# Kernel tuning notes

Measured on AMD Instinct MI355X. Metric: run time of the kernel, lower is better.

Reference implementation:

```python
import jax, jax.numpy as jnp
import numpy as np

B, S, D, H = 2, 2048, 512, 8
DK = D // H


def setup_inputs() -> dict:
    key = jax.random.key(0)
    ks = jax.random.split(key, 6)
    q = jax.random.normal(ks[0], (B, S, D), dtype=jnp.float32)
    k = jax.random.normal(ks[1], (B, S, D), dtype=jnp.float32)
    v = jax.random.normal(ks[2], (B, S, D), dtype=jnp.float32)
    mask = jax.random.randint(ks[3], (1, 1, S, S), 0, 2, dtype=jnp.int32)
    # nn.Linear weights [out, in]; scaled like torch default init
    Wq = jax.random.normal(ks[4], (D, D), dtype=jnp.float32) / np.sqrt(D)
    Wo = jax.random.normal(ks[5], (D, D), dtype=jnp.float32) / np.sqrt(D)
    return {"q": q, "k": k, "v": v, "mask": mask, "Wq": Wq, "Wo": Wo}


def _split_heads(x):
    # [B,S,D] -> [B,H,S,DK]
    return x.reshape(B, S, H, DK).transpose(0, 2, 1, 3)


def reference(q, k, v, mask, Wq, Wo):
    # NOTE: original module applies Wq to q, k AND v (faithful to source bug)
    query = _split_heads(q @ Wq.T)
    key_ = _split_heads(k @ Wq.T)
    value = _split_heads(v @ Wq.T)
    scores = jnp.einsum("bhqd,bhkd->bhqk", query, key_) / np.sqrt(DK).astype(np.float32)
    # original uses masked_fill_(mask==0, 1e-09) BEFORE softmax (not -inf)
    scores = jnp.where(mask == 0, jnp.float32(1e-9), scores)
    attn = jax.nn.softmax(scores, axis=-1)  # dropout p=0.0 -> identity
    x = jnp.einsum("bhqk,bhkd->bhqd", attn, value)
    x = x.transpose(0, 2, 1, 3).reshape(B, S, D)
    return x @ Wo.T
```

## Files before the change

### kernel.cpp

```cpp
#include <hip/hip_runtime.h>
#include <hip/hip_bf16.h>
#include <stdint.h>

#define S_LEN 2048
#define D_MOD 512
#define N_H   8
#define D_K   64

typedef short v8s __attribute__((ext_vector_type(8)));
typedef short v4s __attribute__((ext_vector_type(4)));
typedef float v4f __attribute__((ext_vector_type(4)));

__device__ __forceinline__ short f2bf(float f) {
  union { float f; unsigned u; } a; a.f = f;
  unsigned u = a.u;
  u += 0x7fffu + ((u >> 16) & 1u);
  return (short)(u >> 16);
}

__device__ __forceinline__ v4f mfma16(v8s a, v8s b, v4f c) {
  return __builtin_amdgcn_mfma_f32_16x16x32_bf16(a, b, c, 0, 0, 0);
}

__global__ __launch_bounds__(256) void cvt_kernel(
    const float* __restrict__ q, const float* __restrict__ k,
    const float* __restrict__ v, const float* __restrict__ Wq,
    const float* __restrict__ Wo,
    short* __restrict__ qb, short* __restrict__ kb, short* __restrict__ vb,
    short* __restrict__ Wqb, short* __restrict__ Wob)
{
  unsigned g = blockIdx.x * 256 + threadIdx.x;
  const float* src; short* dst; unsigned off;
  if (g < 524288u)        { src = q;  dst = qb;  off = g; }
  else if (g < 1048576u)  { src = k;  dst = kb;  off = g - 524288u; }
  else if (g < 1572864u)  { src = v;  dst = vb;  off = g - 1048576u; }
  else if (g < 1638400u)  { src = Wq; dst = Wqb; off = g - 1572864u; }
  else                    { src = Wo; dst = Wob; off = g - 1638400u; }
  float4 x = ((const float4*)src)[off];
  v4s p; p.x = f2bf(x.x); p.y = f2bf(x.y); p.z = f2bf(x.z); p.w = f2bf(x.w);
  ((v4s*)dst)[off] = p;
}

__global__ __launch_bounds__(256) void maskpack_kernel(
    const int* __restrict__ mask, unsigned long long* __restrict__ mp)
{
  int id = blockIdx.x * 256 + threadIdx.x;
  const int4* m4 = (const int4*)(mask + (size_t)id * 64);
  unsigned long long w = 0ull;
#pragma unroll
  for (int j = 0; j < 16; j++) {
    int4 v = m4[j];
    w |= (unsigned long long)(v.x != 0) << (j * 4 + 0);
    w |= (unsigned long long)(v.y != 0) << (j * 4 + 1);
    w |= (unsigned long long)(v.z != 0) << (j * 4 + 2);
    w |= (unsigned long long)(v.w != 0) << (j * 4 + 3);
  }
  mp[id] = w;
}

__global__ __launch_bounds__(256) void proj_kernel(
    const short* __restrict__ qb, const short* __restrict__ kb,
    const short* __restrict__ vb, const short* __restrict__ Wqb,
    short* __restrict__ QP, short* __restrict__ KP, short* __restrict__ VT)
{
  const int z = blockIdx.z;
  const short* __restrict__ A = (z == 0) ? qb : ((z == 1) ? kb : vb);
  const int m0 = blockIdx.x * 64, n0 = blockIdx.y * 64;
  const int tid = threadIdx.x;
  const int wave = tid >> 6, lane = tid & 63;
  const int quad = lane >> 4, l15 = lane & 15;
  const int wm = wave >> 1, wn = wave & 1;
  __shared__ short As[64][72];
  __shared__ short Bs[64][72];
  v4f acc[2][2];
#pragma unroll
  for (int i = 0; i < 2; i++)
#pragma unroll
    for (int j = 0; j < 2; j++) acc[i][j] = (v4f){0.f, 0.f, 0.f, 0.f};

  v8s a8[2], b8[2];
#pragma unroll
  for (int i = 0; i < 2; i++) {
    int fi = tid + i * 256, r = fi >> 3, c = (fi & 7) << 3;
    a8[i] = *(const v8s*)&A[(m0 + r) * 512 + c];
    b8[i] = *(const v8s*)&Wqb[(n0 + r) * 512 + c];
  }

  for (int kk = 0; kk < 512; kk += 64) {
    __syncthreads();
#pragma unroll
    for (int i = 0; i < 2; i++) {
      int fi = tid + i * 256, r = fi >> 3, c = (fi & 7) << 3;
      *(v8s*)&As[r][c] = a8[i];
      *(v8s*)&Bs[r][c] = b8[i];
    }
    __syncthreads();
    if (kk + 64 < 512) {
#pragma unroll
      for (int i = 0; i < 2; i++) {
        int fi = tid + i * 256, r = fi >> 3, c = (fi & 7) << 3;
        a8[i] = *(const v8s*)&A[(m0 + r) * 512 + kk + 64 + c];
        b8[i] = *(const v8s*)&Wqb[(n0 + r) * 512 + kk + 64 + c];
      }
    }
#pragma unroll
    for (int ms = 0; ms < 2; ms++)
#pragma unroll
      for (int ns = 0; ns < 2; ns++)
#pragma unroll
        for (int ks = 0; ks < 2; ks++) {
          union { v8s v; v4s h2[2]; } a, bb;
          a.h2[0]  = *(const v4s*)&As[wm * 32 + ms * 16 + l15][ks * 32 + quad * 8];
          a.h2[1]  = *(const v4s*)&As[wm * 32 + ms * 16 + l15][ks * 32 + quad * 8 + 4];
          bb.h2[0] = *(const v4s*)&Bs[wn * 32 + ns * 16 + l15][ks * 32 + quad * 8];
          bb.h2[1] = *(const v4s*)&Bs[wn * 32 + ns * 16 + l15][ks * 32 + quad * 8 + 4];
          acc[ms][ns] = mfma16(a.v, bb.v, acc[ms][ns]);
        }
  }
#pragma unroll
  for (int ms = 0; ms < 2; ms++)
#pragma unroll
    for (int ns = 0; ns < 2; ns++) {
      int mb = m0 + wm * 32 + ms * 16 + quad * 4;
      int n  = n0 + wn * 32 + ns * 16 + l15;
      int bI = mb >> 11, s = mb & 2047, hh = n >> 6, dk = n & 63;
      if (z == 2) {
        v4s pv;
        pv.x = f2bf(acc[ms][ns][0]); pv.y = f2bf(acc[ms][ns][1]);
        pv.z = f2bf(acc[ms][ns][2]); pv.w = f2bf(acc[ms][ns][3]);
        *(v4s*)&VT[((bI * N_H + hh) * D_K + dk) * S_LEN + s] = pv;
      } else {
        short* dst = (z == 0) ? QP : KP;
#pragma unroll
        for (int r = 0; r < 4; r++)
          dst[((bI * N_H + hh) * S_LEN + (s + r)) * D_K + dk] = f2bf(acc[ms][ns][r]);
      }
    }
}

__global__ __launch_bounds__(512, 4) void attn_kernel(
    const short* __restrict__ QP, const short* __restrict__ KP,
    const short* __restrict__ VT, const unsigned long long* __restrict__ mp,
    short* __restrict__ XP)
{
  const int h = blockIdx.y, b = blockIdx.z;
  const int tid = threadIdx.x;
  const int wave = tid >> 6;
  const int half = wave >> 2;
  const int wq   = wave & 3;
  const int lane = tid & 63;
  const int quad = lane >> 4, l15 = lane & 15;
  const short* Qh = QP + ((b * N_H + h) * S_LEN) * D_K;
  const short* Kh = KP + ((b * N_H + h) * S_LEN) * D_K;
  const short* Vh = VT + ((b * N_H + h) * D_K) * S_LEN;

  __shared__ char smem[54272];
  short* Ks = (short*)smem + half * 4608;
  short* Vs = (short*)(smem + 18432) + half * 4608;
  short* Pl = (short*)(smem + 36864) + wave * 1088;
  float* CB = (float*)smem;

  const int qrow = blockIdx.x * 64 + wq * 16;
  const int t8   = tid & 255;
  const int srow = t8 >> 2;
  const int sc   = (t8 & 3) * 8;
  const int ch0  = half * 1024;

  v8s aQ[2];
#pragma unroll
  for (int ks = 0; ks < 2; ks++)
    aQ[ks] = *(const v8s*)&Qh[(qrow + l15) * D_K + ks * 32 + quad * 8];

  const float MASKP = 3.3546263e-4f;
  const v8s ONES = {16256,16256,16256,16256,16256,16256,16256,16256};
  v4f accX[4], accL = (v4f){0.f, 0.f, 0.f, 0.f};
#pragma unroll
  for (int t = 0; t < 4; t++) accX[t] = (v4f){0.f, 0.f, 0.f, 0.f};

  v8s kreg0 = *(const v8s*)&Kh[(ch0 + srow) * D_K + sc];
  v8s kreg1 = *(const v8s*)&Kh[(ch0 + srow) * D_K + sc + 32];
  v8s vreg0 = *(const v8s*)&Vh[srow * S_LEN + ch0 + sc];
  v8s vreg1 = *(const v8s*)&Vh[srow * S_LEN + ch0 + sc + 32];
  unsigned long long mwc[4], mwn[4];
#pragma unroll
  for (int r = 0; r < 4; r++)
    mwc[r] = mp[(qrow + quad * 4 + r) * 32 + half * 16];

  for (int kt = 0; kt < 16; kt++) {
    __syncthreads();
    *(v8s*)&Ks[srow * 72 + sc]      = kreg0;
    *(v8s*)&Ks[srow * 72 + sc + 32] = kreg1;
    *(v8s*)&Vs[srow * 72 + sc]      = vreg0;
    *(v8s*)&Vs[srow * 72 + sc + 32] = vreg1;
    __syncthreads();

    if (kt + 1 < 16) {
      const int c1 = ch0 + (kt + 1) * 64;
      kreg0 = *(const v8s*)&Kh[(c1 + srow) * D_K + sc];
      kreg1 = *(const v8s*)&Kh[(c1 + srow) * D_K + sc + 32];
      vreg0 = *(const v8s*)&Vh[srow * S_LEN + c1 + sc];
      vreg1 = *(const v8s*)&Vh[srow * S_LEN + c1 + sc + 32];
#pragma unroll
      for (int r = 0; r < 4; r++)
        mwn[r] = mp[(qrow + quad * 4 + r) * 32 + half * 16 + kt + 1];
    }

#pragma unroll
    for (int t = 0; t < 4; t++) {
      v4f s = (v4f){0.f, 0.f, 0.f, 0.f};
#pragma unroll
      for (int ks = 0; ks < 2; ks++) {
        v8s bK = *(const v8s*)&Ks[(t * 16 + l15) * 72 + ks * 32 + quad * 8];
        s = mfma16(aQ[ks], bK, s);
      }
#pragma unroll
      for (int r = 0; r < 4; r++) {
        int bit = (int)((mwc[r] >> (t * 16 + l15)) & 1ull);
        float p = bit ? __expf(fmaf(s[r], 0.125f, -8.0f)) : MASKP;
        Pl[(quad * 4 + r) * 68 + t * 16 + l15] = f2bf(p);
      }
    }

    union { v8s v; v4s h2[2]; } aP[2];
#pragma unroll
    for (int ks = 0; ks < 2; ks++) {
      aP[ks].h2[0] = *(const v4s*)&Pl[l15 * 68 + ks * 32 + quad * 8];
      aP[ks].h2[1] = *(const v4s*)&Pl[l15 * 68 + ks * 32 + quad * 8 + 4];
    }
#pragma unroll
    for (int t = 0; t < 4; t++)
#pragma unroll
      for (int ks = 0; ks < 2; ks++) {
        v8s bV = *(const v8s*)&Vs[(t * 16 + l15) * 72 + ks * 32 + quad * 8];
        accX[t] = mfma16(aP[ks].v, bV, accX[t]);
      }
    accL = mfma16(aP[0].v, ONES, accL);
    accL = mfma16(aP[1].v, ONES, accL);

#pragma unroll
    for (int r = 0; r < 4; r++) mwc[r] = mwn[r];
  }

  __syncthreads();
  if (half == 1) {
    float* c = CB + (wq * 64 + lane) * 21;
#pragma unroll
    for (int t = 0; t < 4; t++)
#pragma unroll
      for (int r = 0; r < 4; r++) c[t * 4 + r] = accX[t][r];
#pragma unroll
    for (int r = 0; r < 4; r++) c[16 + r] = accL[r];
  }
  __syncthreads();
  if (half == 0) {
    const float* c = CB + (wq * 64 + lane) * 21;
#pragma unroll
    for (int t = 0; t < 4; t++)
#pragma unroll
      for (int r = 0; r < 4; r++) accX[t][r] += c[t * 4 + r];
    float linv[4];
#pragma unroll
    for (int r = 0; r < 4; r++) linv[r] = 1.0f / (accL[r] + c[16 + r]);
#pragma unroll
    for (int t = 0; t < 4; t++)
#pragma unroll
      for (int r = 0; r < 4; r++) {
        float x = accX[t][r] * linv[r];
        int srw = qrow + quad * 4 + r;
        XP[(b * S_LEN + srw) * D_MOD + h * D_K + t * 16 + l15] = f2bf(x);
      }
  }
}

__global__ __launch_bounds__(256) void outproj_kernel(
    const short* __restrict__ XP, const short* __restrict__ Wob,
    float* __restrict__ out)
{
  const int m0 = blockIdx.x * 64, n0 = blockIdx.y * 64;
  const int tid = threadIdx.x;
  const int wave = tid >> 6, lane = tid & 63;
  const int quad = lane >> 4, l15 = lane & 15;
  const int wm = wave >> 1, wn = wave & 1;
  __shared__ short As[64][72];
  __shared__ short Bs[64][72];
  v4f acc[2][2];
#pragma unroll
  for (int i = 0; i < 2; i++)
#pragma unroll
    for (int j = 0; j < 2; j++) acc[i][j] = (v4f){0.f, 0.f, 0.f, 0.f};

  v8s a8[2], b8[2];
#pragma unroll
  for (int i = 0; i < 2; i++) {
    int fi = tid + i * 256, r = fi >> 3, c = (fi & 7) << 3;
    a8[i] = *(const v8s*)&XP[(m0 + r) * 512 + c];
    b8[i] = *(const v8s*)&Wob[(n0 + r) * 512 + c];
  }

  for (int kk = 0; kk < 512; kk += 64) {
    __syncthreads();
#pragma unroll
    for (int i = 0; i < 2; i++) {
      int fi = tid + i * 256, r = fi >> 3, c = (fi & 7) << 3;
      *(v8s*)&As[r][c] = a8[i];
      *(v8s*)&Bs[r][c] = b8[i];
    }
    __syncthreads();
    if (kk + 64 < 512) {
#pragma unroll
      for (int i = 0; i < 2; i++) {
        int fi = tid + i * 256, r = fi >> 3, c = (fi & 7) << 3;
        a8[i] = *(const v8s*)&XP[(m0 + r) * 512 + kk + 64 + c];
        b8[i] = *(const v8s*)&Wob[(n0 + r) * 512 + kk + 64 + c];
      }
    }
#pragma unroll
    for (int ms = 0; ms < 2; ms++)
#pragma unroll
      for (int ns = 0; ns < 2; ns++)
#pragma unroll
        for (int ks = 0; ks < 2; ks++) {
          union { v8s v; v4s h2[2]; } a, bb;
          a.h2[0]  = *(const v4s*)&As[wm * 32 + ms * 16 + l15][ks * 32 + quad * 8];
          a.h2[1]  = *(const v4s*)&As[wm * 32 + ms * 16 + l15][ks * 32 + quad * 8 + 4];
          bb.h2[0] = *(const v4s*)&Bs[wn * 32 + ns * 16 + l15][ks * 32 + quad * 8];
          bb.h2[1] = *(const v4s*)&Bs[wn * 32 + ns * 16 + l15][ks * 32 + quad * 8 + 4];
          acc[ms][ns] = mfma16(a.v, bb.v, acc[ms][ns]);
        }
  }
#pragma unroll
  for (int ms = 0; ms < 2; ms++)
#pragma unroll
    for (int ns = 0; ns < 2; ns++) {
      int n = n0 + wn * 32 + ns * 16 + l15;
#pragma unroll
      for (int r = 0; r < 4; r++) {
        int m = m0 + wm * 32 + ms * 16 + quad * 4 + r;
        out[m * 512 + n] = acc[ms][ns][r];
      }
    }
}

extern "C" void kernel_launch(void* const* d_in, const int* in_sizes, int n_in,
                              void* d_out, int out_size, void* d_ws, size_t ws_size,
                              hipStream_t stream) {
  const float* q  = (const float*)d_in[0];
  const float* k  = (const float*)d_in[1];
  const float* v  = (const float*)d_in[2];
  const int* mask = (const int*)d_in[3];
  const float* Wq = (const float*)d_in[4];
  const float* Wo = (const float*)d_in[5];
  float* out = (float*)d_out;
  char* ws = (char*)d_ws;
  short* QP = (short*)(ws);
  short* KP = (short*)(ws + (4u << 20));
  short* VT = (short*)(ws + (8u << 20));
  short* XP = (short*)(ws + (12u << 20));
  unsigned long long* MP = (unsigned long long*)(ws + (16u << 20));
  short* qb  = (short*)(ws + (17u << 20));
  short* kb  = (short*)(ws + (21u << 20));
  short* vb  = (short*)(ws + (25u << 20));
  short* Wqb = (short*)(ws + (29u << 20));
  short* Wob = (short*)(ws + (29u << 20) + (512u << 10));

  cvt_kernel<<<dim3(6656), 256, 0, stream>>>(q, k, v, Wq, Wo, qb, kb, vb, Wqb, Wob);
  maskpack_kernel<<<dim3(256), 256, 0, stream>>>(mask, MP);
  proj_kernel<<<dim3(64, 8, 3), 256, 0, stream>>>(qb, kb, vb, Wqb, QP, KP, VT);
  attn_kernel<<<dim3(32, N_H, 2), 512, 0, stream>>>(QP, KP, VT, MP, XP);
  outproj_kernel<<<dim3(64, 8, 1), 256, 0, stream>>>(XP, Wob, out);
}
```

Baseline: 159.7 us.

## Keep softmax probabilities in registers via transposed QK MFMA and merge prep kernels

The attention kernel now computes S^T by swapping the MFMA operands. Each lane therefore holds the probabilities in the layout needed as the A operand of a 16x16x16 bf16 MFMA for the PV product. This removes the per-wave LDS round trip for P. The row sum moves from an MFMA against a ones vector to a scalar accumulation plus cross-lane shuffles, and LDS usage shrinks. Separately, the conversion and mask-packing kernels are merged into a single launch; the trade-off is more, smaller MFMA instructions for PV.

New measurement: 163.8 us. 2.6% more time.

```diff
diff --git a/kernel.cpp b/kernel.cpp
--- a/kernel.cpp
+++ b/kernel.cpp
@@ -21,41 +21,44 @@
 __device__ __forceinline__ v4f mfma16(v8s a, v8s b, v4f c) {
   return __builtin_amdgcn_mfma_f32_16x16x32_bf16(a, b, c, 0, 0, 0);
 }
-
-__global__ __launch_bounds__(256) void cvt_kernel(
+__device__ __forceinline__ v4f mfma16x16(v4s a, v4s b, v4f c) {
+  return __builtin_amdgcn_mfma_f32_16x16x16bf16_1k(a, b, c, 0, 0, 0);
+}
+
+__global__ __launch_bounds__(256) void prep_kernel(
     const float* __restrict__ q, const float* __restrict__ k,
     const float* __restrict__ v, const float* __restrict__ Wq,
-    const float* __restrict__ Wo,
+    const float* __restrict__ Wo, const int* __restrict__ mask,
     short* __restrict__ qb, short* __restrict__ kb, short* __restrict__ vb,
-    short* __restrict__ Wqb, short* __restrict__ Wob)
+    short* __restrict__ Wqb, short* __restrict__ Wob,
+    unsigned long long* __restrict__ mp)
 {
-  unsigned g = blockIdx.x * 256 + threadIdx.x;
-  const float* src; short* dst; unsigned off;
-  if (g < 524288u)        { src = q;  dst = qb;  off = g; }
-  else if (g < 1048576u)  { src = k;  dst = kb;  off = g - 524288u; }
-  else if (g < 1572864u)  { src = v;  dst = vb;  off = g - 1048576u; }
-  else if (g < 1638400u)  { src = Wq; dst = Wqb; off = g - 1572864u; }
-  else                    { src = Wo; dst = Wob; off = g - 1638400u; }
-  float4 x = ((const float4*)src)[off];
-  v4s p; p.x = f2bf(x.x); p.y = f2bf(x.y); p.z = f2bf(x.z); p.w = f2bf(x.w);
-  ((v4s*)dst)[off] = p;
-}
-
-__global__ __launch_bounds__(256) void maskpack_kernel(
-    const int* __restrict__ mask, unsigned long long* __restrict__ mp)
-{
-  int id = blockIdx.x * 256 + threadIdx.x;
-  const int4* m4 = (const int4*)(mask + (size_t)id * 64);
-  unsigned long long w = 0ull;
-#pragma unroll
-  for (int j = 0; j < 16; j++) {
-    int4 v = m4[j];
-    w |= (unsigned long long)(v.x != 0) << (j * 4 + 0);
-    w |= (unsigned long long)(v.y != 0) << (j * 4 + 1);
-    w |= (unsigned long long)(v.z != 0) << (j * 4 + 2);
-    w |= (unsigned long long)(v.w != 0) << (j * 4 + 3);
-  }
-  mp[id] = w;
+  unsigned bx = blockIdx.x;
+  if (bx < 6656u) {
+    unsigned g = bx * 256 + threadIdx.x;
+    const float* src; short* dst; unsigned off;
+    if (g < 524288u)        { src = q;  dst = qb;  off = g; }
+    else if (g < 1048576u)  { src = k;  dst = kb;  off = g - 524288u; }
+    else if (g < 1572864u)  { src = v;  dst = vb;  off = g - 1048576u; }
+    else if (g < 1638400u)  { src = Wq; dst = Wqb; off = g - 1572864u; }
+    else                    { src = Wo; dst = Wob; off = g - 1638400u; }
+    float4 x = ((const float4*)src)[off];
+    v4s p; p.x = f2bf(x.x); p.y = f2bf(x.y); p.z = f2bf(x.z); p.w = f2bf(x.w);
+    ((v4s*)dst)[off] = p;
+  } else {
+    int id = (bx - 6656u) * 256 + threadIdx.x;
+    const int4* m4 = (const int4*)(mask + (size_t)id * 64);
+    unsigned long long w = 0ull;
+#pragma unroll
+    for (int j = 0; j < 16; j++) {
+      int4 mv = m4[j];
+      w |= (unsigned long long)(mv.x != 0) << (j * 4 + 0);
+      w |= (unsigned long long)(mv.y != 0) << (j * 4 + 1);
+      w |= (unsigned long long)(mv.z != 0) << (j * 4 + 2);
+      w |= (unsigned long long)(mv.w != 0) << (j * 4 + 3);
+    }
+    mp[id] = w;
+  }
 }
 
 __global__ __launch_bounds__(256) void proj_kernel(
@@ -154,10 +157,9 @@
   const short* Kh = KP + ((b * N_H + h) * S_LEN) * D_K;
   const short* Vh = VT + ((b * N_H + h) * D_K) * S_LEN;
 
-  __shared__ char smem[54272];
+  __shared__ char smem[36864];
   short* Ks = (short*)smem + half * 4608;
   short* Vs = (short*)(smem + 18432) + half * 4608;
-  short* Pl = (short*)(smem + 36864) + wave * 1088;
   float* CB = (float*)smem;
 
   const int qrow = blockIdx.x * 64 + wq * 16;
@@ -172,19 +174,17 @@
     aQ[ks] = *(const v8s*)&Qh[(qrow + l15) * D_K + ks * 32 + quad * 8];
 
   const float MASKP = 3.3546263e-4f;
-  const v8s ONES = {16256,16256,16256,16256,16256,16256,16256,16256};
-  v4f accX[4], accL = (v4f){0.f, 0.f, 0.f, 0.f};
-#pragma unroll
-  for (int t = 0; t < 4; t++) accX[t] = (v4f){0.f, 0.f, 0.f, 0.f};
+  float lacc = 0.f;
+  v4f accX[4];
+#pragma unroll
+  for (int u = 0; u < 4; u++) accX[u] = (v4f){0.f, 0.f, 0.f, 0.f};
 
   v8s kreg0 = *(const v8s*)&Kh[(ch0 + srow) * D_K + sc];
   v8s kreg1 = *(const v8s*)&Kh[(ch0 + srow) * D_K + sc + 32];
   v8s vreg0 = *(const v8s*)&Vh[srow * S_LEN + ch0 + sc];
   v8s vreg1 = *(const v8s*)&Vh[srow * S_LEN + ch0 + sc + 32];
-  unsigned long long mwc[4], mwn[4];
-#pragma unroll
-  for (int r = 0; r < 4; r++)
-    mwc[r] = mp[(qrow + quad * 4 + r) * 32 + half * 16];
+  unsigned long long mwc = mp[(qrow + l15) * 32 + half * 16];
+  unsigned long long mwn = 0ull;
 
   for (int kt = 0; kt < 16; kt++) {
     __syncthreads();
@@ -200,74 +200,73 @@
       kreg1 = *(const v8s*)&Kh[(c1 + srow) * D_K + sc + 32];
       vreg0 = *(const v8s*)&Vh[srow * S_LEN + c1 + sc];
       vreg1 = *(const v8s*)&Vh[srow * S_LEN + c1 + sc + 32];
-#pragma unroll
-      for (int r = 0; r < 4; r++)
-        mwn[r] = mp[(qrow + quad * 4 + r) * 32 + half * 16 + kt + 1];
-    }
-
-#pragma unroll
-    for (int t = 0; t < 4; t++) {
+      mwn = mp[(qrow + l15) * 32 + half * 16 + kt + 1];
+    }
+
+    v4s pa[4];
+#pragma unroll
+    for (int tp = 0; tp < 4; tp++) {
       v4f s = (v4f){0.f, 0.f, 0.f, 0.f};
 #pragma unroll
       for (int ks = 0; ks < 2; ks++) {
-        v8s bK = *(const v8s*)&Ks[(t * 16 + l15) * 72 + ks * 32 + quad * 8];
-        s = mfma16(aQ[ks], bK, s);
-      }
+        v8s bK = *(const v8s*)&Ks[(tp * 16 + l15) * 72 + ks * 32 + quad * 8];
+        s = mfma16(bK, aQ[ks], s);
+      }
+      v4s pk;
 #pragma unroll
       for (int r = 0; r < 4; r++) {
-        int bit = (int)((mwc[r] >> (t * 16 + l15)) & 1ull);
+        int kap = tp * 16 + quad * 4 + r;
+        int bit = (int)((mwc >> kap) & 1ull);
         float p = bit ? __expf(fmaf(s[r], 0.125f, -8.0f)) : MASKP;
-        Pl[(quad * 4 + r) * 68 + t * 16 + l15] = f2bf(p);
-      }
-    }
-
-    union { v8s v; v4s h2[2]; } aP[2];
-#pragma unroll
-    for (int ks = 0; ks < 2; ks++) {
-      aP[ks].h2[0] = *(const v4s*)&Pl[l15 * 68 + ks * 32 + quad * 8];
-      aP[ks].h2[1] = *(const v4s*)&Pl[l15 * 68 + ks * 32 + quad * 8 + 4];
-    }
-#pragma unroll
-    for (int t = 0; t < 4; t++)
-#pragma unroll
-      for (int ks = 0; ks < 2; ks++) {
-        v8s bV = *(const v8s*)&Vs[(t * 16 + l15) * 72 + ks * 32 + quad * 8];
-        accX[t] = mfma16(aP[ks].v, bV, accX[t]);
-      }
-    accL = mfma16(aP[0].v, ONES, accL);
-    accL = mfma16(aP[1].v, ONES, accL);
-
-#pragma unroll
-    for (int r = 0; r < 4; r++) mwc[r] = mwn[r];
-  }
+        lacc += p;
+        pk[r] = f2bf(p);
+      }
+      pa[tp] = pk;
+    }
+
+#pragma unroll
+    for (int u = 0; u < 4; u++) {
+      const short* vb_ = &Vs[(u * 16 + l15) * 72 + quad * 4];
+#pragma unroll
+      for (int tp = 0; tp < 4; tp++) {
+        v4s bV = *(const v4s*)&vb_[tp * 16];
+        accX[u] = mfma16x16(pa[tp], bV, accX[u]);
+      }
+    }
+    mwc = mwn;
+  }
+
+  lacc += __shfl_xor(lacc, 16);
+  lacc += __shfl_xor(lacc, 32);
 
   __syncthreads();
   if (half == 1) {
-    float* c = CB + (wq * 64 + lane) * 21;
-#pragma unroll
-    for (int t = 0; t < 4; t++)
-#pragma unroll
-      for (int r = 0; r < 4; r++) c[t * 4 + r] = accX[t][r];
-#pragma unroll
-    for (int r = 0; r < 4; r++) c[16 + r] = accL[r];
+    float* c = CB + (wq * 64 + lane) * 17;
+#pragma unroll
+    for (int u = 0; u < 4; u++)
+#pragma unroll
+      for (int r = 0; r < 4; r++) c[u * 4 + r] = accX[u][r];
+    c[16] = lacc;
   }
   __syncthreads();
   if (half == 0) {
-    const float* c = CB + (wq * 64 + lane) * 21;
-#pragma unroll
-    for (int t = 0; t < 4; t++)
-#pragma unroll
-      for (int r = 0; r < 4; r++) accX[t][r] += c[t * 4 + r];
-    float linv[4];
-#pragma unroll
-    for (int r = 0; r < 4; r++) linv[r] = 1.0f / (accL[r] + c[16 + r]);
-#pragma unroll
-    for (int t = 0; t < 4; t++)
+    const float* c = CB + (wq * 64 + lane) * 17;
+#pragma unroll
+    for (int u = 0; u < 4; u++)
+#pragma unroll
+      for (int r = 0; r < 4; r++) accX[u][r] += c[u * 4 + r];
+    float lsum = lacc + c[16];
+    float inv[4];
+#pragma unroll
+    for (int r = 0; r < 4; r++)
+      inv[r] = 1.0f / __shfl(lsum, quad * 4 + r);
+#pragma unroll
+    for (int u = 0; u < 4; u++)
 #pragma unroll
       for (int r = 0; r < 4; r++) {
-        float x = accX[t][r] * linv[r];
+        float x = accX[u][r] * inv[r];
         int srw = qrow + quad * 4 + r;
-        XP[(b * S_LEN + srw) * D_MOD + h * D_K + t * 16 + l15] = f2bf(x);
+        XP[(b * S_LEN + srw) * D_MOD + h * D_K + u * 16 + l15] = f2bf(x);
       }
   }
 }
@@ -363,8 +362,8 @@
   short* Wqb = (short*)(ws + (29u << 20));
   short* Wob = (short*)(ws + (29u << 20) + (512u << 10));
 
-  cvt_kernel<<<dim3(6656), 256, 0, stream>>>(q, k, v, Wq, Wo, qb, kb, vb, Wqb, Wob);
-  maskpack_kernel<<<dim3(256), 256, 0, stream>>>(mask, MP);
+  prep_kernel<<<dim3(6912), 256, 0, stream>>>(q, k, v, Wq, Wo, mask,
+                                              qb, kb, vb, Wqb, Wob, MP);
   proj_kernel<<<dim3(64, 8, 3), 256, 0, stream>>>(qb, kb, vb, Wqb, QP, KP, VT);
   attn_kernel<<<dim3(32, N_H, 2), 512, 0, stream>>>(QP, KP, VT, MP, XP);
   outproj_kernel<<<dim3(64, 8, 1), 256, 0, stream>>>(XP, Wob, out);
```
